# Optimization experiments

Measured on AMD Instinct MI355X. Metric: run time of the kernel, lower is better.

## Reference

```python
import jax, jax.numpy as jnp
import numpy as np

K = 3          # conv kernel size
G = 3          # KAN grid intervals
SPLINE_K = 3   # B-spline order
N_BASIS = G + SPLINE_K  # 6


def extended_grid():
    # pykan-style grid on [-1, 1] with G intervals, extended by k knots each side
    h = 2.0 / G
    return jnp.arange(-SPLINE_K, G + SPLINE_K + 1, dtype=jnp.float32) * h - 1.0  # [G+2k+1]


def bspline_basis(x, t, k):
    """Cox-de Boor recursion. x: [...], t: [m] knots -> [..., m-1-k] bases."""
    x = x[..., None]
    b = ((x >= t[:-1]) & (x < t[1:])).astype(x.dtype)  # degree 0: [..., m-1]
    for d in range(1, k + 1):
        left = (x - t[: -(d + 1)]) / (t[d:-1] - t[: -(d + 1)]) * b[..., :-1]
        right = (t[d + 1:] - x) / (t[d + 1:] - t[1:-d]) * b[..., 1:]
        b = left + right
    return b  # [..., m-1-k]


def setup_inputs() -> dict:
    key = jax.random.key(0)
    k1, k2, k3, k4 = jax.random.split(key, 4)
    B, C, H, W = 32, 16, 64, 64
    in_dim, out_dim = C * K * K, 64
    x = jax.random.normal(k1, (B, C, H, W), dtype=jnp.float32)
    coef = jax.random.normal(k2, (in_dim, out_dim, N_BASIS), dtype=jnp.float32) * 0.1
    scale_base = jax.random.normal(k3, (in_dim, out_dim), dtype=jnp.float32) * (1.0 / np.sqrt(in_dim))
    scale_sp = jnp.ones((in_dim, out_dim), dtype=jnp.float32) + 0.0 * jax.random.normal(k4, (in_dim, out_dim))
    return {"x": x, "coef": coef, "scale_base": scale_base, "scale_sp": scale_sp}


def reference(x, coef, scale_base, scale_sp):
    B, C, H, W = x.shape
    Ho, Wo = H - K + 1, W - K + 1
    # im2col with torch-reshape ordering: feature index = c*K*K + di*K + dj
    cols = [x[:, :, di:di + Ho, dj:dj + Wo] for di in range(K) for dj in range(K)]
    patches = jnp.stack(cols, axis=2)                    # [B, C, K*K, Ho, Wo]
    patches = patches.reshape(B, C * K * K, Ho, Wo)      # [B, D, Ho, Wo]
    p = patches.transpose(0, 2, 3, 1)                    # [B, Ho, Wo, D]

    t = extended_grid()
    basis = bspline_basis(p, t, SPLINE_K)                # [B, Ho, Wo, D, N_BASIS]
    # spline part: sum over input dims and bases, with per-edge scale_sp folded into coef
    spline = jnp.einsum('bhwdn,don->bhwo', basis, coef * scale_sp[:, :, None])
    base = jnp.einsum('bhwd,do->bhwo', jax.nn.silu(p), scale_base)
    y = base + spline                                    # [B, Ho, Wo, O]
    return y.transpose(0, 3, 1, 2)                       # [B, O, Ho, Wo]
```

## Files before the change

### kernel.cpp

```cpp
#include <hip/hip_runtime.h>
#include <math.h>

#define Bsz 32
#define Cc  16
#define Hh  64
#define Ww  64
#define HO  62
#define WO  62
#define OD  64
#define ND  144
#define NCHUNK 36
#define BSKEW 520
#define BSM_U16 77824

using short8 = __attribute__((ext_vector_type(8))) short;
using f32x4  = __attribute__((ext_vector_type(4))) float;

__device__ __forceinline__ unsigned short f2bf(float f) {
    union { float f; unsigned u; } v; v.f = f;
    unsigned r = v.u + 0x7fff + ((v.u >> 16) & 1);
    return (unsigned short)(r >> 16);
}
__device__ __forceinline__ float bf2f(unsigned short h) {
    union { unsigned u; float f; } v; v.u = ((unsigned)h) << 16; return v.f;
}

__device__ __forceinline__ uint4 feat_pack(float xv) {
    float xi = (xv + 3.0f) * 1.5f;
    float fi = floorf(xi);
    int   ii = (int)fi;
    float u  = xi - fi;
    float u2 = u * u, u3 = u2 * u;
    float P0 = u3 * (1.0f / 6.0f);
    float P1 = (1.0f + 3.0f * u + 3.0f * u2 - 3.0f * u3) * (1.0f / 6.0f);
    float P2 = (4.0f - 6.0f * u2 + 3.0f * u3) * (1.0f / 6.0f);
    float om = 1.0f - u;
    float P3 = om * om * om * (1.0f / 6.0f);
    bool ok = (ii >= 0) && (ii <= 8);
    float bas[6];
    #pragma unroll
    for (int n = 0; n < 6; ++n) {
        int t = ii - n;
        float v = (t == 0) ? P0 : (t == 1) ? P1 : (t == 2) ? P2 : (t == 3) ? P3 : 0.0f;
        bas[n] = ok ? v : 0.0f;
    }
    float s = xv / (1.0f + __expf(-xv));
    unsigned short sh = f2bf(s);
    unsigned short sl = f2bf(s - bf2f(sh));
    uint4 pk;
    pk.x = (unsigned)f2bf(bas[0]) | ((unsigned)f2bf(bas[1]) << 16);
    pk.y = (unsigned)f2bf(bas[2]) | ((unsigned)f2bf(bas[3]) << 16);
    pk.z = (unsigned)f2bf(bas[4]) | ((unsigned)f2bf(bas[5]) << 16);
    pk.w = (unsigned)sh | ((unsigned)sl << 16);
    return pk;
}

__global__ __launch_bounds__(256) void kan_feat(const float* __restrict__ x,
                                                const float* __restrict__ coef,
                                                const float* __restrict__ sbase,
                                                const float* __restrict__ ssp,
                                                uint4* __restrict__ fg,
                                                unsigned short* __restrict__ wps) {
    const int bid = blockIdx.x, tid = threadIdx.x;
    if (bid < 1024) {
        #pragma unroll
        for (int p = 0; p < 2; ++p) {
            int e0 = bid * 2048 + p * 1024 + tid * 4;
            float4 xv = *(const float4*)&x[e0];
            fg[e0 + 0] = feat_pack(xv.x);
            fg[e0 + 1] = feat_pack(xv.y);
            fg[e0 + 2] = feat_pack(xv.z);
            fg[e0 + 3] = feat_pack(xv.w);
        }
    } else {
        int g = (bid - 1024) * 256 + tid;
        if (g >= BSM_U16 / 8) return;
        int p8   = g * 8;
        int dd   = p8 / BSKEW;
        int rem8 = (p8 - dd * BSKEW) >> 3;
        unsigned short v8[8];
        #pragma unroll
        for (int n = 0; n < 8; ++n) v8[n] = 0;
        if (dd < ND && rem8 < 64) {
            int o = rem8;
            float sspv = ssp[dd * OD + o];
            #pragma unroll
            for (int n = 0; n < 6; ++n) v8[n] = f2bf(coef[(dd * OD + o) * 6 + n] * sspv);
            unsigned short sb = f2bf(sbase[dd * OD + o]);
            v8[6] = sb; v8[7] = sb;
        }
        uint4 pk;
        pk.x = (unsigned)v8[0] | ((unsigned)v8[1] << 16);
        pk.y = (unsigned)v8[2] | ((unsigned)v8[3] << 16);
        pk.z = (unsigned)v8[4] | ((unsigned)v8[5] << 16);
        pk.w = (unsigned)v8[6] | ((unsigned)v8[7] << 16);
        *(uint4*)&wps[p8] = pk;
    }
}

__global__ __launch_bounds__(512) void kan_gemm(const uint4* __restrict__ fg,
                                                const unsigned short* __restrict__ wps,
                                                float* __restrict__ out) {
    __shared__ unsigned short bsm[BSM_U16];

    const int tid  = threadIdx.x;
    const int bb   = blockIdx.x >> 3;
    const int wid  = tid >> 6;
    const int h    = (blockIdx.x & 7) * 8 + wid;
    const int lane = tid & 63;
    const int l15  = lane & 15;
    const int ks   = lane >> 4;
    const bool alive = (h < HO);

    {
        const uint4* src = (const uint4*)wps;
        uint4* dst = (uint4*)bsm;
        #pragma unroll
        for (int it = 0; it < 19; ++it) dst[it * 512 + tid] = src[it * 512 + tid];
    }
    __syncthreads();

    f32x4 acc[4][4];
    #pragma unroll
    for (int rt = 0; rt < 4; ++rt)
        #pragma unroll
        for (int ct = 0; ct < 4; ++ct) acc[rt][ct] = (f32x4){0.f, 0.f, 0.f, 0.f};

    if (alive) {
        const unsigned short* bbase = bsm + ks * BSKEW + l15 * 8;

        auto loadA = [&](int cb, short8* A) {
            int dd  = cb * 4 + ks;
            int c   = (dd * 57) >> 9;
            int rem = dd - c * 9;
            int di  = (rem * 11) >> 5;
            int dj  = rem - di * 3;
            const short8* ap = (const short8*)fg + ((((bb * Cc + c) << 6) + h + di) << 6) + l15 + dj;
            A[0] = ap[0]; A[1] = ap[16]; A[2] = ap[32]; A[3] = ap[48];
        };
        auto loadB = [&](int cb, short8* Bf) {
            const short8* bp = (const short8*)(bbase + cb * 4 * BSKEW);
            Bf[0] = bp[0]; Bf[1] = bp[16]; Bf[2] = bp[32]; Bf[3] = bp[48];
        };
        auto mfmas = [&](short8* Ax, short8* Bx) {
            #pragma unroll
            for (int rt = 0; rt < 4; ++rt)
                #pragma unroll
                for (int ct = 0; ct < 4; ++ct)
                    acc[rt][ct] = __builtin_amdgcn_mfma_f32_16x16x32_bf16(Ax[rt], Bx[ct], acc[rt][ct], 0, 0, 0);
        };

        short8 A0[4], A1[4], A2[4], B0[4], B1[4];
        loadA(0, A0); loadA(1, A1); loadA(2, A2);
        loadB(0, B0); loadB(1, B1);

        for (int cb = 0; cb < NCHUNK; cb += 6) {
            mfmas(A0, B0);
            if (cb + 3 < NCHUNK) loadA(cb + 3, A0);
            if (cb + 2 < NCHUNK) loadB(cb + 2, B0);
            mfmas(A1, B1);
            if (cb + 4 < NCHUNK) loadA(cb + 4, A1);
            if (cb + 3 < NCHUNK) loadB(cb + 3, B1);
            mfmas(A2, B0);
            if (cb + 5 < NCHUNK) loadA(cb + 5, A2);
            if (cb + 4 < NCHUNK) loadB(cb + 4, B0);
            mfmas(A0, B1);
            if (cb + 6 < NCHUNK) loadA(cb + 6, A0);
            if (cb + 5 < NCHUNK) loadB(cb + 5, B1);
            mfmas(A1, B0);
            if (cb + 7 < NCHUNK) loadA(cb + 7, A1);
            if (cb + 6 < NCHUNK) loadB(cb + 6, B0);
            mfmas(A2, B1);
            if (cb + 8 < NCHUNK) loadA(cb + 8, A2);
            if (cb + 7 < NCHUNK) loadB(cb + 7, B1);
        }
    }

    __syncthreads();
    if (alive) {
        float* sc = (float*)bsm + wid * (OD * 68);
        #pragma unroll
        for (int rt = 0; rt < 4; ++rt)
            #pragma unroll
            for (int ct = 0; ct < 4; ++ct)
                *(f32x4*)&sc[(ct * 16 + l15) * 68 + rt * 16 + ks * 4] = acc[rt][ct];

        const int jh = lane >> 5;
        const int r  = lane & 31;
        #pragma unroll 8
        for (int it = 0; it < 32; ++it) {
            int j = it * 2 + jh;
            if (r < 31) {
                float2 v = *(float2*)&sc[j * 68 + r * 2];
                *(float2*)&out[((bb * OD + j) * HO + h) * WO + r * 2] = v;
            }
        }
    }
}

#define FW 68
__global__ __launch_bounds__(256) void kan_prep(const float* __restrict__ coef,
                                                const float* __restrict__ sbase,
                                                const float* __restrict__ ssp,
                                                unsigned short* __restrict__ wp) {
    int idx = blockIdx.x * 256 + threadIdx.x;
    if (idx >= ND * OD * 8) return;
    int n = idx & 7, o = (idx >> 3) & 63, d = idx >> 9;
    float v = (n < 6) ? coef[(d * OD + o) * 6 + n] * ssp[d * OD + o] : sbase[d * OD + o];
    wp[idx] = f2bf(v);
}

__global__ __launch_bounds__(128) void kan_mfma(const float* __restrict__ x,
                                                const unsigned short* __restrict__ wp,
                                                float* __restrict__ out) {
    __shared__ uint4 feat[Cc * 4 * FW];
    const int rp = blockIdx.x, b = blockIdx.y, tid = threadIdx.x;
    const int wid = tid >> 6, lane = tid & 63, l15 = lane & 15, ks = lane >> 4;
    const int hrow0 = rp * 2;
    for (int i = tid; i < Cc * 4 * FW; i += 128) {
        int wl = i % FW, cr = i / FW, r = cr & 3, c = cr >> 2;
        int col = wl < Ww ? wl : Ww - 1;
        feat[i] = feat_pack(x[((b * Cc + c) * Hh + hrow0 + r) * Ww + col]);
    }
    __syncthreads();
    f32x4 acc[4][4];
    #pragma unroll
    for (int rt = 0; rt < 4; ++rt)
        #pragma unroll
        for (int ct = 0; ct < 4; ++ct) acc[rt][ct] = (f32x4){0.f, 0.f, 0.f, 0.f};
    auto loadA = [&](int chunk, short8* A) {
        int d = chunk * 4 + ks;
        int c = (d * 57) >> 9;
        int rem = d - c * 9;
        int di = (rem * 11) >> 5;
        int dj = rem - di * 3;
        const short8* ap = (const short8*)&feat[(c * 4 + wid + di) * FW + l15 + dj];
        A[0] = ap[0]; A[1] = ap[16]; A[2] = ap[32]; A[3] = ap[48];
    };
    auto loadB = [&](int chunk, short8* Bf) {
        int d = chunk * 4 + ks;
        const short8* bp = (const short8*)wp + (d * 64 + l15);
        Bf[0] = bp[0]; Bf[1] = bp[16]; Bf[2] = bp[32]; Bf[3] = bp[48];
    };
    short8 A0[4], B0[4], A1[4], B1[4];
    loadA(0, A0); loadB(0, B0);
    for (int cb = 0; cb < NCHUNK; cb += 2) {
        loadA(cb + 1, A1); loadB(cb + 1, B1);
        #pragma unroll
        for (int rt = 0; rt < 4; ++rt)
            #pragma unroll
            for (int ct = 0; ct < 4; ++ct)
                acc[rt][ct] = __builtin_amdgcn_mfma_f32_16x16x32_bf16(A0[rt], B0[ct], acc[rt][ct], 0, 0, 0);
        if (cb + 2 < NCHUNK) { loadA(cb + 2, A0); loadB(cb + 2, B0); }
        #pragma unroll
        for (int rt = 0; rt < 4; ++rt)
            #pragma unroll
            for (int ct = 0; ct < 4; ++ct)
                acc[rt][ct] = __builtin_amdgcn_mfma_f32_16x16x32_bf16(A1[rt], B1[ct], acc[rt][ct], 0, 0, 0);
    }
    __syncthreads();
    float* sC = ((float*)feat) + wid * (OD * FW);
    #pragma unroll
    for (int rt = 0; rt < 4; ++rt)
        #pragma unroll
        for (int ct = 0; ct < 4; ++ct)
            *(f32x4*)&sC[(ct * 16 + l15) * FW + rt * 16 + ks * 4] = acc[rt][ct];
    const int orow = hrow0 + wid;
    for (int j = 0; j < OD; ++j) {
        float v = sC[j * FW + lane];
        if (lane < WO) out[((b * OD + j) * HO + orow) * WO + lane] = v;
    }
}

extern "C" void kernel_launch(void* const* d_in, const int* in_sizes, int n_in,
                              void* d_out, int out_size, void* d_ws, size_t ws_size,
                              hipStream_t stream) {
    (void)in_sizes; (void)n_in; (void)out_size;
    const float* x     = (const float*)d_in[0];
    const float* coef  = (const float*)d_in[1];
    const float* sbase = (const float*)d_in[2];
    const float* ssp   = (const float*)d_in[3];
    float* out = (float*)d_out;

    const size_t wps_bytes   = (size_t)BSM_U16 * 2;
    const size_t featg_bytes = (size_t)Bsz * Cc * Hh * Ww * 16;
    const size_t need = wps_bytes + featg_bytes + 64;

    if (ws_size >= need) {
        unsigned short* wps = (unsigned short*)d_ws;
        uint4* fg = (uint4*)((char*)d_ws + wps_bytes);
        kan_feat<<<1024 + 38, 256, 0, stream>>>(x, coef, sbase, ssp, fg, wps);
        kan_gemm<<<256, 512, 0, stream>>>(fg, wps, out);
    } else if (ws_size >= (size_t)ND * OD * 8 * 2) {
        unsigned short* wp = (unsigned short*)d_ws;
        kan_prep<<<(ND * OD * 8 + 255) / 256, 256, 0, stream>>>(coef, sbase, ssp, wp);
        dim3 grid(HO / 2, Bsz);
        kan_mfma<<<grid, 128, 0, stream>>>(x, wp, out);
    }
}
```

Before: 54.65 us.

## Remap K-dimension so each lane group reads one channel, double-buffer loads, direct stores

The weight packing now assigns input dims so that lane group ks handles channels ks*4..ks*4+3 across chunks, which simplifies A addressing to a fixed base plus cb-derived offsets. Block indexing is swizzled so consecutive blocks cover different batches, which may spread memory traffic. The main loop switches to a fully unrolled double-buffer that loads two chunks ahead. The epilogue writes accumulators straight to global memory, dropping the LDS transpose and the barrier, at the cost of less coalesced stores and higher register pressure.

```diff
diff --git a/kernel.cpp b/kernel.cpp
--- a/kernel.cpp
+++ b/kernel.cpp
@@ -63,9 +63,10 @@
                                                 unsigned short* __restrict__ wps) {
     const int bid = blockIdx.x, tid = threadIdx.x;
     if (bid < 1024) {
+        const int bb = bid & 31, part = bid >> 5;
         #pragma unroll
         for (int p = 0; p < 2; ++p) {
-            int e0 = bid * 2048 + p * 1024 + tid * 4;
+            int e0 = (bb * 32 + part) * 2048 + p * 1024 + tid * 4;
             float4 xv = *(const float4*)&x[e0];
             fg[e0 + 0] = feat_pack(xv.x);
             fg[e0 + 1] = feat_pack(xv.y);
@@ -76,17 +77,18 @@
         int g = (bid - 1024) * 256 + tid;
         if (g >= BSM_U16 / 8) return;
         int p8   = g * 8;
-        int dd   = p8 / BSKEW;
-        int rem8 = (p8 - dd * BSKEW) >> 3;
+        int slot = p8 / BSKEW;
+        int o    = (p8 - slot * BSKEW) >> 3;
         unsigned short v8[8];
         #pragma unroll
         for (int n = 0; n < 8; ++n) v8[n] = 0;
-        if (dd < ND && rem8 < 64) {
-            int o = rem8;
-            float sspv = ssp[dd * OD + o];
-            #pragma unroll
-            for (int n = 0; n < 6; ++n) v8[n] = f2bf(coef[(dd * OD + o) * 6 + n] * sspv);
-            unsigned short sb = f2bf(sbase[dd * OD + o]);
+        if (slot < ND && o < 64) {
+            int cb = slot >> 2, ks = slot & 3;
+            int dsrc = ks * 36 + cb;
+            float sspv = ssp[dsrc * OD + o];
+            #pragma unroll
+            for (int n = 0; n < 6; ++n) v8[n] = f2bf(coef[(dsrc * OD + o) * 6 + n] * sspv);
+            unsigned short sb = f2bf(sbase[dsrc * OD + o]);
             v8[6] = sb; v8[7] = sb;
         }
         uint4 pk;
@@ -104,9 +106,11 @@
     __shared__ unsigned short bsm[BSM_U16];
 
     const int tid  = threadIdx.x;
-    const int bb   = blockIdx.x >> 3;
+    const int bid  = blockIdx.x;
+    const int bb   = bid & 31;
+    const int hg   = bid >> 5;
     const int wid  = tid >> 6;
-    const int h    = (blockIdx.x & 7) * 8 + wid;
+    const int h    = hg * 8 + wid;
     const int lane = tid & 63;
     const int l15  = lane & 15;
     const int ks   = lane >> 4;
@@ -127,22 +131,20 @@
         for (int ct = 0; ct < 4; ++ct) acc[rt][ct] = (f32x4){0.f, 0.f, 0.f, 0.f};
 
     if (alive) {
+        const short8* awbase = (const short8*)fg +
+            (((size_t)(bb * Cc + ks * 4) * 64 + h) << 6) + l15;
         const unsigned short* bbase = bsm + ks * BSKEW + l15 * 8;
 
         auto loadA = [&](int cb, short8* A) {
-            int dd  = cb * 4 + ks;
-            int c   = (dd * 57) >> 9;
-            int rem = dd - c * 9;
-            int di  = (rem * 11) >> 5;
-            int dj  = rem - di * 3;
-            const short8* ap = (const short8*)fg + ((((bb * Cc + c) << 6) + h + di) << 6) + l15 + dj;
+            const int cc = cb / 9, rem = cb % 9, di = rem / 3, dj = rem % 3;
+            const short8* ap = awbase + ((cc * 64 + di) * 64 + dj);
             A[0] = ap[0]; A[1] = ap[16]; A[2] = ap[32]; A[3] = ap[48];
         };
         auto loadB = [&](int cb, short8* Bf) {
             const short8* bp = (const short8*)(bbase + cb * 4 * BSKEW);
             Bf[0] = bp[0]; Bf[1] = bp[16]; Bf[2] = bp[32]; Bf[3] = bp[48];
         };
-        auto mfmas = [&](short8* Ax, short8* Bx) {
+        auto mfmas = [&](const short8* Ax, const short8* Bx) {
             #pragma unroll
             for (int rt = 0; rt < 4; ++rt)
                 #pragma unroll
@@ -150,49 +152,30 @@
                     acc[rt][ct] = __builtin_amdgcn_mfma_f32_16x16x32_bf16(Ax[rt], Bx[ct], acc[rt][ct], 0, 0, 0);
         };
 
-        short8 A0[4], A1[4], A2[4], B0[4], B1[4];
-        loadA(0, A0); loadA(1, A1); loadA(2, A2);
-        loadB(0, B0); loadB(1, B1);
-
-        for (int cb = 0; cb < NCHUNK; cb += 6) {
-            mfmas(A0, B0);
-            if (cb + 3 < NCHUNK) loadA(cb + 3, A0);
-            if (cb + 2 < NCHUNK) loadB(cb + 2, B0);
-            mfmas(A1, B1);
-            if (cb + 4 < NCHUNK) loadA(cb + 4, A1);
-            if (cb + 3 < NCHUNK) loadB(cb + 3, B1);
-            mfmas(A2, B0);
-            if (cb + 5 < NCHUNK) loadA(cb + 5, A2);
-            if (cb + 4 < NCHUNK) loadB(cb + 4, B0);
-            mfmas(A0, B1);
-            if (cb + 6 < NCHUNK) loadA(cb + 6, A0);
-            if (cb + 5 < NCHUNK) loadB(cb + 5, B1);
-            mfmas(A1, B0);
-            if (cb + 7 < NCHUNK) loadA(cb + 7, A1);
-            if (cb + 6 < NCHUNK) loadB(cb + 6, B0);
-            mfmas(A2, B1);
-            if (cb + 8 < NCHUNK) loadA(cb + 8, A2);
-            if (cb + 7 < NCHUNK) loadB(cb + 7, B1);
-        }
-    }
-
-    __syncthreads();
-    if (alive) {
-        float* sc = (float*)bsm + wid * (OD * 68);
-        #pragma unroll
-        for (int rt = 0; rt < 4; ++rt)
-            #pragma unroll
-            for (int ct = 0; ct < 4; ++ct)
-                *(f32x4*)&sc[(ct * 16 + l15) * 68 + rt * 16 + ks * 4] = acc[rt][ct];
-
-        const int jh = lane >> 5;
-        const int r  = lane & 31;
-        #pragma unroll 8
-        for (int it = 0; it < 32; ++it) {
-            int j = it * 2 + jh;
-            if (r < 31) {
-                float2 v = *(float2*)&sc[j * 68 + r * 2];
-                *(float2*)&out[((bb * OD + j) * HO + h) * WO + r * 2] = v;
+        short8 Aa[8], Ba[8], Ab[8], Bb[8];
+        loadA(0, Aa); loadA(1, Aa + 4); loadB(0, Ba); loadB(1, Ba + 4);
+
+        #pragma unroll
+        for (int s = 0; s < 18; ++s) {
+            if ((s & 1) == 0) {
+                if (s < 17) { loadA(2*s+2, Ab); loadA(2*s+3, Ab+4); loadB(2*s+2, Bb); loadB(2*s+3, Bb+4); }
+                mfmas(Aa, Ba); mfmas(Aa + 4, Ba + 4);
+            } else {
+                if (s < 17) { loadA(2*s+2, Aa); loadA(2*s+3, Aa+4); loadB(2*s+2, Ba); loadB(2*s+3, Ba+4); }
+                mfmas(Ab, Bb); mfmas(Ab + 4, Bb + 4);
+            }
+        }
+
+        #pragma unroll
+        for (int ct = 0; ct < 4; ++ct) {
+            const int o = ct * 16 + l15;
+            float* orow = out + (((size_t)(bb * OD + o) * HO + h) * WO);
+            #pragma unroll
+            for (int rt = 0; rt < 4; ++rt) {
+                const int w0 = rt * 16 + ks * 4;
+                f32x4 v = acc[rt][ct];
+                *(float2*)(orow + w0) = (float2){v.x, v.y};
+                if (w0 + 2 < WO) *(float2*)(orow + w0 + 2) = (float2){v.z, v.w};
             }
         }
     }
```

Result: faster. 51.38 us (-6.0%).
